# Optimization experiments

Measured on AMD Instinct MI355X. Metric: run time of the kernel, lower is better.

## Reference

```python
import jax, jax.numpy as jnp
import numpy as np

N_USER = 100000
N_ITEM = 50000
N = N_USER + N_ITEM
E = 2400000
D = 64
L = 3
B = 4096
NEG_SLOPE = 0.01  # nn.LeakyReLU() default


def setup_inputs() -> dict:
    key = jax.random.key(0)
    ks = jax.random.split(key, 12)
    return {
        "features": jax.random.normal(ks[0], (N, D), dtype=jnp.float32),
        "rows": jax.random.randint(ks[1], (E,), 0, N),
        "cols": jax.random.randint(ks[2], (E,), 0, N),
        "vals": jax.random.uniform(ks[3], (E,), dtype=jnp.float32) * 0.02,
        "users": jax.random.randint(ks[4], (B,), 0, N_USER),
        "items": jax.random.randint(ks[5], (B,), 0, N_ITEM),
        "W1": jax.random.normal(ks[6], (L, D, D), dtype=jnp.float32) * 0.1,
        "b1": jax.random.normal(ks[7], (L, D), dtype=jnp.float32) * 0.01,
        "W2": jax.random.normal(ks[8], (L, D, D), dtype=jnp.float32) * 0.1,
        "b2": jax.random.normal(ks[9], (L, D), dtype=jnp.float32) * 0.01,
        "Wt": jax.random.normal(ks[10], (D, (L + 1) * D), dtype=jnp.float32) * 0.05,
        "bt": jax.random.normal(ks[11], (D,), dtype=jnp.float32) * 0.01,
    }


def _spmm(rows, cols, vals, x):
    # COO SpMM: out[r] += vals[e] * x[cols[e]]
    msgs = vals[:, None] * x[cols]  # [E, D] gather + scale
    return jax.ops.segment_sum(msgs, rows, num_segments=N)


def reference(features, rows, cols, vals, users, items, W1, b1, W2, b2, Wt, bt):
    feats = features
    embs = [feats]
    for l in range(L):
        agg = _spmm(rows, cols, vals, feats)          # sparse.mm(graph, features)
        part1 = (agg + feats) @ W1[l].T + b1[l]       # (graph+selfLoop) @ f -> Linear
        part2 = (agg * feats) @ W2[l].T + b2[l]       # elementwise mul -> Linear
        feats = jax.nn.leaky_relu(part1 + part2, negative_slope=NEG_SLOPE)
        embs.append(feats)
    final_emb = jnp.concatenate(embs, axis=1)         # [N, (L+1)*D]
    user_emb = final_emb[users] @ Wt.T + bt           # [B, D]
    item_emb = final_emb[N_USER + items] @ Wt.T + bt  # [B, D]
    return jnp.sum(user_emb * item_emb, axis=1)       # [B]
```

## Files before the change

kernel.cpp:

```cpp
#include <hip/hip_runtime.h>

#define N_USER 100000
#define N_NODE 150000
#define N_EDGE 2400000
#define DIM 64
#define BPAIR 4096
#define NEG_SLOPE 0.01f


__global__ void count_kernel(const int* __restrict__ rows, int* __restrict__ cnt) {
    int i = blockIdx.x * blockDim.x + threadIdx.x;
    if (i < N_EDGE) atomicAdd(&cnt[rows[i]], 1);
}

__global__ void scan1_kernel(const int* __restrict__ cnt, int* __restrict__ incl,
                             int* __restrict__ bsums) {
    __shared__ int s[256];
    int t = threadIdx.x;
    int i = blockIdx.x * 256 + t;
    s[t] = (i < N_NODE) ? cnt[i] : 0;
    __syncthreads();
    for (int off = 1; off < 256; off <<= 1) {
        int add = (t >= off) ? s[t - off] : 0;
        __syncthreads();
        s[t] += add;
        __syncthreads();
    }
    if (i < N_NODE) incl[i] = s[t];
    if (t == 255) bsums[blockIdx.x] = s[255];
}

__global__ void scan2_kernel(int* __restrict__ bsums, int nblk) {
    __shared__ int s[1024];
    int t = threadIdx.x;
    s[t] = (t < nblk) ? bsums[t] : 0;
    __syncthreads();
    for (int off = 1; off < 1024; off <<= 1) {
        int add = (t >= off) ? s[t - off] : 0;
        __syncthreads();
        s[t] += add;
        __syncthreads();
    }
    if (t < nblk) bsums[t] = s[t];
}

__global__ void scan3_kernel(int* __restrict__ row_ptr, const int* __restrict__ bsums) {
    int i = blockIdx.x * 256 + threadIdx.x;
    if (i == 0) row_ptr[0] = 0;
    if (i < N_NODE && blockIdx.x > 0) row_ptr[1 + i] += bsums[blockIdx.x - 1];
}

__global__ void scatter_kernel(const int* __restrict__ rows, const int* __restrict__ cols,
                               const float* __restrict__ vals, const int* __restrict__ row_ptr,
                               int* __restrict__ cursor, int* __restrict__ col_s,
                               float* __restrict__ val_s) {
    int i = blockIdx.x * blockDim.x + threadIdx.x;
    if (i < N_EDGE) {
        int r = rows[i];
        int p = row_ptr[r] + atomicAdd(&cursor[r], 1);
        col_s[p] = cols[i];
        val_s[p] = vals[i];
    }
}

__global__ __launch_bounds__(256) void layer_kernel(
    const int* __restrict__ row_ptr, const int* __restrict__ col_s,
    const float* __restrict__ val_s, const float* __restrict__ fin,
    float* __restrict__ fout,
    const float* __restrict__ W1l, const float* __restrict__ b1l,
    const float* __restrict__ W2l, const float* __restrict__ b2l) {
    __shared__ float w1t[64][65];
    __shared__ float w2t[64][65];
    __shared__ float h1s[4][64];
    __shared__ float h2s[4][64];
    int t = threadIdx.x;
    for (int idx = t; idx < 4096; idx += 256) {
        int d = idx >> 6, k = idx & 63;
        w1t[k][d] = W1l[idx];
        w2t[k][d] = W2l[idx];
    }
    __syncthreads();
    int wave = t >> 6, lane = t & 63;
    int gwave = (blockIdx.x * 256 + t) >> 6;
    int nwave = (gridDim.x * 256) >> 6;
    float bsum = b1l[lane] + b2l[lane];
    for (int r = gwave; r < N_NODE; r += nwave) {
        int e0 = row_ptr[r], e1 = row_ptr[r + 1];
        float acc = 0.f;
        int j = e0;
        for (; j + 3 < e1; j += 4) {
            int c0 = col_s[j], c1 = col_s[j + 1], c2 = col_s[j + 2], c3 = col_s[j + 3];
            float v0 = val_s[j], v1 = val_s[j + 1], v2 = val_s[j + 2], v3 = val_s[j + 3];
            acc += v0 * fin[(size_t)c0 * DIM + lane];
            acc += v1 * fin[(size_t)c1 * DIM + lane];
            acc += v2 * fin[(size_t)c2 * DIM + lane];
            acc += v3 * fin[(size_t)c3 * DIM + lane];
        }
        for (; j < e1; ++j)
            acc += val_s[j] * fin[(size_t)col_s[j] * DIM + lane];
        float f = fin[(size_t)r * DIM + lane];
        float h1 = acc + f;
        float h2 = acc * f;
        h1s[wave][lane] = h1;
        h2s[wave][lane] = h2;
        float o = bsum;
#pragma unroll 8
        for (int k = 0; k < 64; ++k) {
            o += w1t[k][lane] * h1s[wave][k] + w2t[k][lane] * h2s[wave][k];
        }
        o = (o > 0.f) ? o : NEG_SLOPE * o;
        fout[(size_t)r * DIM + lane] = o;
    }
}

__global__ void gather_kernel(float* __restrict__ dst, const float* __restrict__ src,
                              const int* __restrict__ users, const int* __restrict__ items) {
    int t = threadIdx.x;
    int p = blockIdx.x * 4 + (t >> 6);
    int lane = t & 63;
    if (p < 2 * BPAIR) {
        int node = (p < BPAIR) ? users[p] : (N_USER + items[p - BPAIR]);
        dst[(size_t)p * DIM + lane] = src[(size_t)node * DIM + lane];
    }
}

__global__ void transpose_wt_kernel(const float* __restrict__ Wt, float* __restrict__ wtT) {
    int i = blockIdx.x * 256 + threadIdx.x;
    int d = i >> 8, k = i & 255;
    wtT[k * 64 + d] = Wt[i];
}

__global__ __launch_bounds__(256) void score_kernel(
    const float* __restrict__ features, const float* __restrict__ sel,
    const int* __restrict__ users, const int* __restrict__ items,
    const float* __restrict__ wtT, const float* __restrict__ bt,
    float* __restrict__ out) {
    __shared__ float hu[4][256];
    __shared__ float hv[4][256];
    int t = threadIdx.x;
    int wave = t >> 6, lane = t & 63;
    int gwave = (blockIdx.x * 256 + t) >> 6;
    int nwave = (gridDim.x * 256) >> 6;
    float btv = bt[lane];
    for (int p = gwave; p < BPAIR; p += nwave) {
        int u = users[p];
        int v = N_USER + items[p];
        hu[wave][lane] = features[(size_t)u * DIM + lane];
        hv[wave][lane] = features[(size_t)v * DIM + lane];
        for (int l = 0; l < 3; ++l) {
            hu[wave][64 + l * 64 + lane] = sel[((size_t)l * 2 * BPAIR + p) * DIM + lane];
            hv[wave][64 + l * 64 + lane] = sel[((size_t)l * 2 * BPAIR + BPAIR + p) * DIM + lane];
        }
        float pu = btv, pv = btv;
#pragma unroll 4
        for (int k = 0; k < 256; ++k) {
            float w = wtT[k * 64 + lane];
            pu += w * hu[wave][k];
            pv += w * hv[wave][k];
        }
        float s = pu * pv;
        for (int m = 32; m >= 1; m >>= 1) s += __shfl_xor(s, m, 64);
        if (lane == 0) out[p] = s;
    }
}

extern "C" void kernel_launch(void* const* d_in, const int* in_sizes, int n_in,
                              void* d_out, int out_size, void* d_ws, size_t ws_size,
                              hipStream_t stream) {
    const float* features = (const float*)d_in[0];
    const int*   rows     = (const int*)d_in[1];
    const int*   cols     = (const int*)d_in[2];
    const float* vals     = (const float*)d_in[3];
    const int*   users    = (const int*)d_in[4];
    const int*   items    = (const int*)d_in[5];
    const float* W1       = (const float*)d_in[6];
    const float* b1       = (const float*)d_in[7];
    const float* W2       = (const float*)d_in[8];
    const float* b2       = (const float*)d_in[9];
    const float* Wt       = (const float*)d_in[10];
    const float* bt       = (const float*)d_in[11];
    float* out = (float*)d_out;

    char* ws = (char*)d_ws;
    size_t off = 0;
    auto alloc = [&](size_t bytes) -> void* {
        void* p = ws + off;
        off += (bytes + 255) & ~(size_t)255;
        return p;
    };
    int*   row_ptr = (int*)alloc((N_NODE + 1) * sizeof(int));
    int*   cnt     = (int*)alloc(N_NODE * sizeof(int));
    int*   cursor  = (int*)alloc(N_NODE * sizeof(int));
    int*   bsums   = (int*)alloc(4096);
    int*   col_s   = (int*)alloc(N_EDGE * sizeof(int));
    float* val_s   = (float*)alloc(N_EDGE * sizeof(float));
    float* f0      = (float*)alloc((size_t)N_NODE * DIM * sizeof(float));
    float* f1      = (float*)alloc((size_t)N_NODE * DIM * sizeof(float));
    float* sel     = (float*)alloc((size_t)3 * 2 * BPAIR * DIM * sizeof(float));
    float* wtT     = (float*)alloc(256 * 64 * sizeof(float));

    hipMemsetAsync(cnt, 0, 2 * (((size_t)N_NODE * sizeof(int) + 255) & ~(size_t)255), stream);

    int eblocks = (N_EDGE + 255) / 256;
    int nblk = (N_NODE + 255) / 256;
    count_kernel<<<eblocks, 256, 0, stream>>>(rows, cnt);
    scan1_kernel<<<nblk, 256, 0, stream>>>(cnt, row_ptr + 1, bsums);
    scan2_kernel<<<1, 1024, 0, stream>>>(bsums, nblk);
    scan3_kernel<<<nblk, 256, 0, stream>>>(row_ptr, bsums);
    scatter_kernel<<<eblocks, 256, 0, stream>>>(rows, cols, vals, row_ptr, cursor, col_s, val_s);
    transpose_wt_kernel<<<64, 256, 0, stream>>>(Wt, wtT);

    const float* fin = features;
    float* fbuf[2] = {f0, f1};
    for (int l = 0; l < 3; ++l) {
        float* fout = fbuf[l & 1];
        layer_kernel<<<2048, 256, 0, stream>>>(row_ptr, col_s, val_s, fin, fout,
                                               W1 + (size_t)l * DIM * DIM, b1 + (size_t)l * DIM,
                                               W2 + (size_t)l * DIM * DIM, b2 + (size_t)l * DIM);
        gather_kernel<<<(2 * BPAIR) / 4, 256, 0, stream>>>(sel + (size_t)l * 2 * BPAIR * DIM,
                                                           fout, users, items);
        fin = fout;
    }
    score_kernel<<<256, 256, 0, stream>>>(features, sel, users, items, wtT, bt, out);
}
```

Measured before the change: 1.066 ms.

## Pack edges as int2, unroll gather by 8, use readlane for layer matvec

```diff
diff --git a/kernel.cpp b/kernel.cpp
--- a/kernel.cpp
+++ b/kernel.cpp
@@ -52,64 +52,73 @@
 
 __global__ void scatter_kernel(const int* __restrict__ rows, const int* __restrict__ cols,
                                const float* __restrict__ vals, const int* __restrict__ row_ptr,
-                               int* __restrict__ cursor, int* __restrict__ col_s,
-                               float* __restrict__ val_s) {
+                               int* __restrict__ cursor, int2* __restrict__ edges) {
     int i = blockIdx.x * blockDim.x + threadIdx.x;
     if (i < N_EDGE) {
         int r = rows[i];
         int p = row_ptr[r] + atomicAdd(&cursor[r], 1);
-        col_s[p] = cols[i];
-        val_s[p] = vals[i];
-    }
-}
-
-__global__ __launch_bounds__(256) void layer_kernel(
-    const int* __restrict__ row_ptr, const int* __restrict__ col_s,
-    const float* __restrict__ val_s, const float* __restrict__ fin,
-    float* __restrict__ fout,
+        edges[p] = make_int2(cols[i], __float_as_int(vals[i]));
+    }
+}
+
+__global__ __launch_bounds__(512, 8) void layer_kernel(
+    const int* __restrict__ row_ptr, const int2* __restrict__ edges,
+    const float* __restrict__ fin, float* __restrict__ fout,
     const float* __restrict__ W1l, const float* __restrict__ b1l,
     const float* __restrict__ W2l, const float* __restrict__ b2l) {
-    __shared__ float w1t[64][65];
-    __shared__ float w2t[64][65];
-    __shared__ float h1s[4][64];
-    __shared__ float h2s[4][64];
-    int t = threadIdx.x;
-    for (int idx = t; idx < 4096; idx += 256) {
+    __shared__ float w1t[64][64];
+    __shared__ float w2t[64][64];
+    int t = threadIdx.x;
+    for (int idx = t; idx < 4096; idx += 512) {
         int d = idx >> 6, k = idx & 63;
         w1t[k][d] = W1l[idx];
         w2t[k][d] = W2l[idx];
     }
     __syncthreads();
-    int wave = t >> 6, lane = t & 63;
-    int gwave = (blockIdx.x * 256 + t) >> 6;
-    int nwave = (gridDim.x * 256) >> 6;
+    int lane = t & 63;
+    int gwave = (blockIdx.x * 512 + t) >> 6;
+    int nwave = (gridDim.x * 512) >> 6;
     float bsum = b1l[lane] + b2l[lane];
     for (int r = gwave; r < N_NODE; r += nwave) {
         int e0 = row_ptr[r], e1 = row_ptr[r + 1];
-        float acc = 0.f;
+        float f = fin[((size_t)r << 6) | lane];
+        float a0 = 0.f, a1 = 0.f;
         int j = e0;
-        for (; j + 3 < e1; j += 4) {
-            int c0 = col_s[j], c1 = col_s[j + 1], c2 = col_s[j + 2], c3 = col_s[j + 3];
-            float v0 = val_s[j], v1 = val_s[j + 1], v2 = val_s[j + 2], v3 = val_s[j + 3];
-            acc += v0 * fin[(size_t)c0 * DIM + lane];
-            acc += v1 * fin[(size_t)c1 * DIM + lane];
-            acc += v2 * fin[(size_t)c2 * DIM + lane];
-            acc += v3 * fin[(size_t)c3 * DIM + lane];
-        }
-        for (; j < e1; ++j)
-            acc += val_s[j] * fin[(size_t)col_s[j] * DIM + lane];
-        float f = fin[(size_t)r * DIM + lane];
+        for (; j + 7 < e1; j += 8) {
+            int2 e[8];
+#pragma unroll
+            for (int u = 0; u < 8; ++u) e[u] = edges[j + u];
+            float g[8];
+#pragma unroll
+            for (int u = 0; u < 8; ++u) g[u] = fin[((size_t)e[u].x << 6) | lane];
+#pragma unroll
+            for (int u = 0; u < 8; ++u) {
+                float v = __int_as_float(e[u].y);
+                if (u & 1) a1 += v * g[u]; else a0 += v * g[u];
+            }
+        }
+        for (; j < e1; ++j) {
+            int2 e = edges[j];
+            a0 += __int_as_float(e.y) * fin[((size_t)e.x << 6) | lane];
+        }
+        float acc = a0 + a1;
         float h1 = acc + f;
         float h2 = acc * f;
-        h1s[wave][lane] = h1;
-        h2s[wave][lane] = h2;
-        float o = bsum;
-#pragma unroll 8
-        for (int k = 0; k < 64; ++k) {
-            o += w1t[k][lane] * h1s[wave][k] + w2t[k][lane] * h2s[wave][k];
-        }
+        float o0 = bsum, o1 = 0.f, o2 = 0.f, o3 = 0.f;
+#pragma unroll
+        for (int k = 0; k < 64; k += 2) {
+            float h1a = __int_as_float(__builtin_amdgcn_readlane(__float_as_int(h1), k));
+            float h2a = __int_as_float(__builtin_amdgcn_readlane(__float_as_int(h2), k));
+            float h1b = __int_as_float(__builtin_amdgcn_readlane(__float_as_int(h1), k + 1));
+            float h2b = __int_as_float(__builtin_amdgcn_readlane(__float_as_int(h2), k + 1));
+            o0 += h1a * w1t[k][lane];
+            o1 += h2a * w2t[k][lane];
+            o2 += h1b * w1t[k + 1][lane];
+            o3 += h2b * w2t[k + 1][lane];
+        }
+        float o = (o0 + o1) + (o2 + o3);
         o = (o > 0.f) ? o : NEG_SLOPE * o;
-        fout[(size_t)r * DIM + lane] = o;
+        fout[((size_t)r << 6) | lane] = o;
     }
 }
 
@@ -120,20 +129,14 @@
     int lane = t & 63;
     if (p < 2 * BPAIR) {
         int node = (p < BPAIR) ? users[p] : (N_USER + items[p - BPAIR]);
-        dst[(size_t)p * DIM + lane] = src[(size_t)node * DIM + lane];
-    }
-}
-
-__global__ void transpose_wt_kernel(const float* __restrict__ Wt, float* __restrict__ wtT) {
-    int i = blockIdx.x * 256 + threadIdx.x;
-    int d = i >> 8, k = i & 255;
-    wtT[k * 64 + d] = Wt[i];
+        dst[((size_t)p << 6) | lane] = src[((size_t)node << 6) | lane];
+    }
 }
 
 __global__ __launch_bounds__(256) void score_kernel(
     const float* __restrict__ features, const float* __restrict__ sel,
     const int* __restrict__ users, const int* __restrict__ items,
-    const float* __restrict__ wtT, const float* __restrict__ bt,
+    const float* __restrict__ Wt, const float* __restrict__ bt,
     float* __restrict__ out) {
     __shared__ float hu[4][256];
     __shared__ float hv[4][256];
@@ -142,23 +145,31 @@
     int gwave = (blockIdx.x * 256 + t) >> 6;
     int nwave = (gridDim.x * 256) >> 6;
     float btv = bt[lane];
+    const float4* wrow = (const float4*)(Wt + (size_t)lane * 256);
     for (int p = gwave; p < BPAIR; p += nwave) {
         int u = users[p];
         int v = N_USER + items[p];
-        hu[wave][lane] = features[(size_t)u * DIM + lane];
-        hv[wave][lane] = features[(size_t)v * DIM + lane];
+        hu[wave][lane] = features[((size_t)u << 6) | lane];
+        hv[wave][lane] = features[((size_t)v << 6) | lane];
+#pragma unroll
         for (int l = 0; l < 3; ++l) {
-            hu[wave][64 + l * 64 + lane] = sel[((size_t)l * 2 * BPAIR + p) * DIM + lane];
-            hv[wave][64 + l * 64 + lane] = sel[((size_t)l * 2 * BPAIR + BPAIR + p) * DIM + lane];
-        }
-        float pu = btv, pv = btv;
-#pragma unroll 4
-        for (int k = 0; k < 256; ++k) {
-            float w = wtT[k * 64 + lane];
-            pu += w * hu[wave][k];
-            pv += w * hv[wave][k];
-        }
-        float s = pu * pv;
+            hu[wave][64 + l * 64 + lane] = sel[(((size_t)l * 2 * BPAIR + p) << 6) | lane];
+            hv[wave][64 + l * 64 + lane] = sel[(((size_t)l * 2 * BPAIR + BPAIR + p) << 6) | lane];
+        }
+        const float4* hu4 = (const float4*)&hu[wave][0];
+        const float4* hv4 = (const float4*)&hv[wave][0];
+        float pu0 = btv, pu1 = 0.f, pv0 = btv, pv1 = 0.f;
+#pragma unroll 8
+        for (int kk = 0; kk < 64; ++kk) {
+            float4 w = wrow[kk];
+            float4 a = hu4[kk];
+            float4 b = hv4[kk];
+            pu0 += w.x * a.x + w.z * a.z;
+            pu1 += w.y * a.y + w.w * a.w;
+            pv0 += w.x * b.x + w.z * b.z;
+            pv1 += w.y * b.y + w.w * b.w;
+        }
+        float s = (pu0 + pu1) * (pv0 + pv1);
         for (int m = 32; m >= 1; m >>= 1) s += __shfl_xor(s, m, 64);
         if (lane == 0) out[p] = s;
     }
@@ -192,12 +203,10 @@
     int*   cnt     = (int*)alloc(N_NODE * sizeof(int));
     int*   cursor  = (int*)alloc(N_NODE * sizeof(int));
     int*   bsums   = (int*)alloc(4096);
-    int*   col_s   = (int*)alloc(N_EDGE * sizeof(int));
-    float* val_s   = (float*)alloc(N_EDGE * sizeof(float));
+    int2*  edges   = (int2*)alloc((size_t)N_EDGE * sizeof(int2));
     float* f0      = (float*)alloc((size_t)N_NODE * DIM * sizeof(float));
     float* f1      = (float*)alloc((size_t)N_NODE * DIM * sizeof(float));
     float* sel     = (float*)alloc((size_t)3 * 2 * BPAIR * DIM * sizeof(float));
-    float* wtT     = (float*)alloc(256 * 64 * sizeof(float));
 
     hipMemsetAsync(cnt, 0, 2 * (((size_t)N_NODE * sizeof(int) + 255) & ~(size_t)255), stream);
 
@@ -207,19 +216,18 @@
     scan1_kernel<<<nblk, 256, 0, stream>>>(cnt, row_ptr + 1, bsums);
     scan2_kernel<<<1, 1024, 0, stream>>>(bsums, nblk);
     scan3_kernel<<<nblk, 256, 0, stream>>>(row_ptr, bsums);
-    scatter_kernel<<<eblocks, 256, 0, stream>>>(rows, cols, vals, row_ptr, cursor, col_s, val_s);
-    transpose_wt_kernel<<<64, 256, 0, stream>>>(Wt, wtT);
+    scatter_kernel<<<eblocks, 256, 0, stream>>>(rows, cols, vals, row_ptr, cursor, edges);
 
     const float* fin = features;
     float* fbuf[2] = {f0, f1};
     for (int l = 0; l < 3; ++l) {
         float* fout = fbuf[l & 1];
-        layer_kernel<<<2048, 256, 0, stream>>>(row_ptr, col_s, val_s, fin, fout,
+        layer_kernel<<<2048, 512, 0, stream>>>(row_ptr, edges, fin, fout,
                                                W1 + (size_t)l * DIM * DIM, b1 + (size_t)l * DIM,
                                                W2 + (size_t)l * DIM * DIM, b2 + (size_t)l * DIM);
         gather_kernel<<<(2 * BPAIR) / 4, 256, 0, stream>>>(sel + (size_t)l * 2 * BPAIR * DIM,
                                                            fout, users, items);
         fin = fout;
     }
-    score_kernel<<<256, 256, 0, stream>>>(features, sel, users, items, wtT, bt, out);
-}
+    score_kernel<<<256, 256, 0, stream>>>(features, sel, users, items, Wt, bt, out);
+}
```

Result: slower. 3.175 ms (+197.9%).
